# Optimization experiments

Measured on AMD Instinct MI355X. Metric: run time of the kernel, lower is better.

The kernel has to match this reference:

```python
import jax, jax.numpy as jnp
import numpy as np

D_MODEL = 1024
NUM_HEADS = 16
DEPTH = D_MODEL // NUM_HEADS
NEG_INF = -1e9


def setup_inputs() -> dict:
    key = jax.random.key(0)
    ks = jax.random.split(key, 12)
    B, S = 4, 2048
    scale = 1.0 / np.sqrt(D_MODEL)
    inp = {
        "q": jax.random.normal(ks[0], (B, S, D_MODEL), jnp.float32),
        "k": jax.random.normal(ks[1], (B, S, D_MODEL), jnp.float32),
        "v": jax.random.normal(ks[2], (B, S, D_MODEL), jnp.float32),
        "mask": jax.random.randint(ks[3], (B, 1, 1, S), 0, 2, jnp.int32),
        "wq": jax.random.normal(ks[4], (D_MODEL, D_MODEL), jnp.float32) * scale,
        "bq": jnp.zeros((D_MODEL,), jnp.float32),
        "wk": jax.random.normal(ks[5], (D_MODEL, D_MODEL), jnp.float32) * scale,
        "bk": jnp.zeros((D_MODEL,), jnp.float32),
        "wv": jax.random.normal(ks[6], (D_MODEL, D_MODEL), jnp.float32) * scale,
        "bv": jnp.zeros((D_MODEL,), jnp.float32),
        "wo": jax.random.normal(ks[7], (D_MODEL, D_MODEL), jnp.float32) * scale,
        "bo": jnp.zeros((D_MODEL,), jnp.float32),
    }
    return inp


def _split_heads(x):
    # [B, S, D] -> [B, H, S, depth]
    B, S, _ = x.shape
    return x.reshape(B, S, NUM_HEADS, DEPTH).transpose(0, 2, 1, 3)


def reference(q, k, v, mask, wq, bq, wk, bk, wv, bv, wo, bo):
    B, S, _ = q.shape
    qh = _split_heads(q @ wq + bq)  # [B,H,S,d]
    kh = _split_heads(k @ wk + bk)
    vh = _split_heads(v @ wv + bv)
    logits = jnp.einsum("bhqd,bhkd->bhqk", qh, kh) / jnp.sqrt(
        jnp.asarray(DEPTH, jnp.float32))
    logits = logits + mask.astype(jnp.float32) * NEG_INF
    weights = jax.nn.softmax(logits, axis=-1)
    attn = jnp.einsum("bhqk,bhkd->bhqd", weights, vh)
    attn = attn.transpose(0, 2, 1, 3).reshape(B, S, D_MODEL)
    return attn @ wo + bo
```

## Files before the change

### kernel.cpp

```cpp
#include <hip/hip_runtime.h>

#define SB 4
#define SS 2048
#define SD 1024
#define SH 16

typedef float f32x4 __attribute__((ext_vector_type(4)));
typedef __bf16 bf16x8 __attribute__((ext_vector_type(8)));
typedef short short4v __attribute__((ext_vector_type(4)));
typedef unsigned int uint2v __attribute__((ext_vector_type(2)));

__device__ __forceinline__ unsigned short f2bf_(float x) {
    unsigned u = __builtin_bit_cast(unsigned, x);
    unsigned r = u + 0x7FFFu + ((u >> 16) & 1u);
    return (unsigned short)(r >> 16);
}

#define GL2LDS(g, l) __builtin_amdgcn_global_load_lds( \
    (const __attribute__((address_space(1))) unsigned int*)(g), \
    (__attribute__((address_space(3))) unsigned int*)(l), 16, 0, 0)

__global__ __launch_bounds__(256) void maskprep(
        const int* __restrict__ mk, float* __restrict__ MA, int n) {
    int i = blockIdx.x * 256 + threadIdx.x;
    if (i < n)
        MA[i] = (float)mk[i] * (-1e9f * 1.4426950408889634f) - 8.0f;
}

__global__ __launch_bounds__(256) void transpose4(
        const float* __restrict__ w0, const float* __restrict__ w1,
        const float* __restrict__ w2, const float* __restrict__ w3,
        unsigned short* __restrict__ out) {
    __shared__ unsigned short tile[32][33];
    int zz = blockIdx.z;
    const float* src = (zz == 0) ? w0 : (zz == 1) ? w1 : (zz == 2) ? w2 : w3;
    unsigned short* dst = out + (size_t)zz * 1024 * 1024;
    int x = blockIdx.x * 32 + threadIdx.x;
    int y0 = blockIdx.y * 32;
    for (int j = threadIdx.y; j < 32; j += 8)
        tile[j][threadIdx.x] = f2bf_(src[(size_t)(y0 + j) * 1024 + x]);
    __syncthreads();
    int ox = y0 + threadIdx.x;
    int oy0 = blockIdx.x * 32;
    for (int j = threadIdx.y; j < 32; j += 8)
        dst[(size_t)(oy0 + j) * 1024 + ox] = tile[threadIdx.x][j];
}

__global__ __launch_bounds__(256) void gemm_qkv(
        const float* __restrict__ Aq, const float* __restrict__ Ak,
        const float* __restrict__ Avv, const unsigned short* __restrict__ WT,
        const float* __restrict__ bq, const float* __restrict__ bk,
        const float* __restrict__ bv, unsigned short* __restrict__ Qh,
        unsigned short* __restrict__ Kh, unsigned short* __restrict__ VTr,
        float qscl) {
    const int K = 1024, N = 1024;
    __shared__ alignas(16) float Asmf[2][128][32];
    __shared__ alignas(16) unsigned short Bsm[2][128][32];
    const int zone = blockIdx.z;
    const float* Af = (zone == 0) ? Aq : (zone == 1) ? Ak : Avv;
    const unsigned short* BT = WT + (size_t)zone * 1048576;
    const float* bias = (zone == 0) ? bq : (zone == 1) ? bk : bv;

    const int m0 = blockIdx.x * 128, n0 = blockIdx.y * 128;
    const int lane = threadIdx.x & 63, wid = threadIdx.x >> 6;
    const int wr = wid >> 1, wc = wid & 1;
    const int cl = lane & 15, kg = lane >> 4;

    f32x4 acc[4][4] = {};

    auto STAGE = [&](int buf, int k0) {
#pragma unroll
        for (int i = 0; i < 4; ++i) {
            int base = i * 32 + wid * 8;
            int row = base + (lane >> 3);
            int cs = (lane & 7) ^ (row & 7);
            GL2LDS(Af + (size_t)(m0 + row) * K + k0 + cs * 4, &Asmf[buf][base][0]);
        }
#pragma unroll
        for (int i = 0; i < 2; ++i) {
            int base = (i * 4 + wid) * 16;
            int row = base + (lane >> 2);
            int cs = (lane & 3) ^ ((row >> 1) & 3);
            GL2LDS(BT + (size_t)(n0 + row) * K + k0 + cs * 8, &Bsm[buf][base][0]);
        }
    };

    STAGE(0, 0);
    __syncthreads();

    for (int k0 = 0; k0 < K; k0 += 32) {
        int cur = (k0 >> 5) & 1;
        if (k0 + 32 < K) STAGE(cur ^ 1, k0 + 32);

        bf16x8 af[4], bfv[4];
#pragma unroll
        for (int mi = 0; mi < 4; ++mi) {
            int r = wr * 64 + mi * 16 + cl;
            const float* Ar = &Asmf[cur][r][0];
            f32x4 a0 = *(const f32x4*)(Ar + ((2 * kg) ^ (r & 7)) * 4);
            f32x4 a1 = *(const f32x4*)(Ar + ((2 * kg + 1) ^ (r & 7)) * 4);
#pragma unroll
            for (int e = 0; e < 4; ++e) {
                af[mi][e] = (__bf16)a0[e];
                af[mi][4 + e] = (__bf16)a1[e];
            }
        }
#pragma unroll
        for (int ni = 0; ni < 4; ++ni) {
            int r = wc * 64 + ni * 16 + cl;
            bfv[ni] = *(const bf16x8*)&Bsm[cur][r][(kg ^ ((r >> 1) & 3)) * 8];
        }
#pragma unroll
        for (int mi = 0; mi < 4; ++mi)
#pragma unroll
            for (int ni = 0; ni < 4; ++ni)
                acc[mi][ni] = __builtin_amdgcn_mfma_f32_16x16x32_bf16(
                    af[mi], bfv[ni], acc[mi][ni], 0, 0, 0);
        __syncthreads();
    }

    const int rl = (lane >> 4) * 4;
    float os = (zone == 0) ? qscl : 1.0f;
#pragma unroll
    for (int mi = 0; mi < 4; ++mi) {
#pragma unroll
        for (int ni = 0; ni < 4; ++ni) {
            int row = m0 + wr * 64 + mi * 16 + rl;
            int col = n0 + wc * 64 + ni * 16 + cl;
            float bvv = bias[col];
            f32x4 v = acc[mi][ni];
            if (zone < 2) {
                unsigned short* C = (zone == 0) ? Qh : Kh;
#pragma unroll
                for (int j = 0; j < 4; ++j)
                    C[(size_t)(row + j) * N + col] = f2bf_((v[j] + bvv) * os);
            } else {
                int bb = row >> 11, s = row & 2047;
                short4v pk;
#pragma unroll
                for (int j = 0; j < 4; ++j)
                    pk[j] = (short)f2bf_(v[j] + bvv);
                *(short4v*)&VTr[((size_t)(bb * 1024 + col)) * 2048 + s] = pk;
            }
        }
    }
}

__global__ __launch_bounds__(256) void gemm_out(
        const unsigned short* __restrict__ Ab, const unsigned short* __restrict__ BT,
        const float* __restrict__ bias, float* __restrict__ C,
        int M, int N, int K) {
    __shared__ alignas(16) unsigned short Asmb[2][128][32];
    __shared__ alignas(16) unsigned short Bsm[2][128][32];
    const int m0 = blockIdx.x * 128, n0 = blockIdx.y * 128;
    const int lane = threadIdx.x & 63, wid = threadIdx.x >> 6;
    const int wr = wid >> 1, wc = wid & 1;
    const int cl = lane & 15, kg = lane >> 4;

    f32x4 acc[4][4] = {};

    auto STAGE = [&](int buf, int k0) {
#pragma unroll
        for (int i = 0; i < 2; ++i) {
            int base = (i * 4 + wid) * 16;
            int row = base + (lane >> 2);
            int cs = (lane & 3) ^ ((row >> 1) & 3);
            GL2LDS(Ab + (size_t)(m0 + row) * K + k0 + cs * 8, &Asmb[buf][base][0]);
            GL2LDS(BT + (size_t)(n0 + row) * K + k0 + cs * 8, &Bsm[buf][base][0]);
        }
    };

    STAGE(0, 0);
    __syncthreads();

    for (int k0 = 0; k0 < K; k0 += 32) {
        int cur = (k0 >> 5) & 1;
        if (k0 + 32 < K) STAGE(cur ^ 1, k0 + 32);

        bf16x8 af[4], bfv[4];
#pragma unroll
        for (int mi = 0; mi < 4; ++mi) {
            int r = wr * 64 + mi * 16 + cl;
            af[mi] = *(const bf16x8*)&Asmb[cur][r][(kg ^ ((r >> 1) & 3)) * 8];
        }
#pragma unroll
        for (int ni = 0; ni < 4; ++ni) {
            int r = wc * 64 + ni * 16 + cl;
            bfv[ni] = *(const bf16x8*)&Bsm[cur][r][(kg ^ ((r >> 1) & 3)) * 8];
        }
#pragma unroll
        for (int mi = 0; mi < 4; ++mi)
#pragma unroll
            for (int ni = 0; ni < 4; ++ni)
                acc[mi][ni] = __builtin_amdgcn_mfma_f32_16x16x32_bf16(
                    af[mi], bfv[ni], acc[mi][ni], 0, 0, 0);
        __syncthreads();
    }

    const int rl = (lane >> 4) * 4;
#pragma unroll
    for (int mi = 0; mi < 4; ++mi) {
#pragma unroll
        for (int ni = 0; ni < 4; ++ni) {
            int row = m0 + wr * 64 + mi * 16 + rl;
            int col = n0 + wc * 64 + ni * 16 + cl;
            float bv = bias[col];
            f32x4 v = acc[mi][ni];
#pragma unroll
            for (int j = 0; j < 4; ++j)
                C[(size_t)(row + j) * N + col] = v[j] + bv;
        }
    }
}

__global__ __launch_bounds__(512, 4) void attn_kernel(
        const unsigned short* __restrict__ Qp, const unsigned short* __restrict__ Kp,
        const unsigned short* __restrict__ VT, const float* __restrict__ MA,
        unsigned short* __restrict__ O) {
    __shared__ alignas(16) unsigned short Klds[2][128][64];
    __shared__ alignas(16) unsigned short Vlds[2][64][128];
    const int lane = threadIdx.x & 63, wid = threadIdx.x >> 6;
    const int bh = blockIdx.x;
    const int b = bh >> 4, h = bh & 15;
    const int qt = blockIdx.y;
    const int qrow0 = qt * 256 + wid * 32;
    const int cl = lane & 15, kg = lane >> 4;

    bf16x8 qf[2][2];
#pragma unroll
    for (int qh = 0; qh < 2; ++qh)
#pragma unroll
        for (int kh = 0; kh < 2; ++kh)
            qf[qh][kh] = *(const bf16x8*)&Qp[(size_t)(b * SS + qrow0 + qh * 16 + cl) * SD
                                            + h * 64 + kh * 32 + kg * 8];

    const float* MAb = MA + b * SS;

    bf16x8 onesf;
#pragma unroll
    for (int e = 0; e < 8; ++e) onesf[e] = (__bf16)1.0f;

    f32x4 oacc[2][4] = {};
    f32x4 lacc[2] = {};

    auto STAGE = [&](int buf, int tt) {
        int kt = (tt & 15) * 128;
        {
            int r8 = lane >> 3, c8 = lane & 7;
#pragma unroll
            for (int i = 0; i < 2; ++i) {
                int r = i * 64 + wid * 8 + r8;
                int cs = c8 ^ (r & 7);
                GL2LDS(Kp + (size_t)(b * SS + kt + r) * SD + h * 64 + cs * 8,
                       &Klds[buf][i * 64 + wid * 8][0]);
            }
        }
        {
            int r16 = lane >> 4, c16 = lane & 15;
#pragma unroll
            for (int i = 0; i < 2; ++i) {
                int r = i * 32 + wid * 4 + r16;
                int cs = (c16 & 8) | ((c16 & 7) ^ (r & 7));
                GL2LDS(VT + (size_t)(b * 1024 + h * 64 + r) * 2048 + kt + cs * 8,
                       &Vlds[buf][i * 32 + wid * 4][0]);
            }
        }
    };

    auto QKCOL = [&](int buf, int kt, int cf, f32x4* sv) {
        int r = cf * 16 + cl;
        bf16x8 kf0 = *(const bf16x8*)&Klds[buf][r][((0 + kg) ^ (r & 7)) * 8];
        bf16x8 kf1 = *(const bf16x8*)&Klds[buf][r][((4 + kg) ^ (r & 7)) * 8];
        f32x4 M = *(const f32x4*)&MAb[kt + cf * 16 + 4 * kg];
        __builtin_amdgcn_s_setprio(1);
#pragma unroll
        for (int qh = 0; qh < 2; ++qh) {
            f32x4 s = {};
            s = __builtin_amdgcn_mfma_f32_16x16x32_bf16(kf0, qf[qh][0], s, 0, 0, 0);
            s = __builtin_amdgcn_mfma_f32_16x16x32_bf16(kf1, qf[qh][1], s, 0, 0, 0);
#pragma unroll
            for (int j = 0; j < 4; ++j)
                s[j] = __builtin_amdgcn_exp2f(s[j] + M[j]);
            sv[qh] = s;
        }
        __builtin_amdgcn_s_setprio(0);
    };

    auto STEP = [&](int buf, int t) {
        int kt = t * 128;
#pragma unroll
        for (int ks = 0; ks < 4; ++ks) {
            f32x4 sA[2], sB[2];
            QKCOL(buf, kt, ks, sA);
            QKCOL(buf, kt, ks + 4, sB);
            bf16x8 pa[2];
#pragma unroll
            for (int qh = 0; qh < 2; ++qh) {
                pa[qh][0] = (__bf16)sA[qh][0];
                pa[qh][1] = (__bf16)sA[qh][1];
                pa[qh][2] = (__bf16)sA[qh][2];
                pa[qh][3] = (__bf16)sA[qh][3];
                pa[qh][4] = (__bf16)sB[qh][0];
                pa[qh][5] = (__bf16)sB[qh][1];
                pa[qh][6] = (__bf16)sB[qh][2];
                pa[qh][7] = (__bf16)sB[qh][3];
            }
            __builtin_amdgcn_s_setprio(1);
#pragma unroll
            for (int qh = 0; qh < 2; ++qh)
                lacc[qh] = __builtin_amdgcn_mfma_f32_16x16x32_bf16(
                    pa[qh], onesf, lacc[qh], 0, 0, 0);
#pragma unroll
            for (int nf = 0; nf < 4; ++nf) {
                int d = nf * 16 + cl;
                int c16a = 2 * ks + (kg >> 1);
                int c16b = 2 * (ks + 4) + (kg >> 1);
                int cha = (c16a & 8) | ((c16a & 7) ^ (d & 7));
                int chb = (c16b & 8) | ((c16b & 7) ^ (d & 7));
                const char* vb = (const char*)&Vlds[buf][d][0];
                uint2v lo = *(const uint2v*)(vb + cha * 16 + (kg & 1) * 8);
                uint2v hi = *(const uint2v*)(vb + chb * 16 + (kg & 1) * 8);
                bf16x8 vf;
                *(uint2v*)&vf = lo;
                *((uint2v*)&vf + 1) = hi;
#pragma unroll
                for (int qh = 0; qh < 2; ++qh)
                    oacc[qh][nf] = __builtin_amdgcn_mfma_f32_16x16x32_bf16(
                        pa[qh], vf, oacc[qh][nf], 0, 0, 0);
            }
            __builtin_amdgcn_s_setprio(0);
        }
    };

    STAGE(0, 0);
    __syncthreads();
    for (int t = 0; t < 16; ++t) {
        int cur = t & 1;
        STAGE(cur ^ 1, t + 1);
        STEP(cur, t);
        __syncthreads();
    }

#pragma unroll
    for (int qh = 0; qh < 2; ++qh) {
#pragma unroll
        for (int j = 0; j < 4; ++j) {
            float inv = 1.0f / lacc[qh][j];
#pragma unroll
            for (int nf = 0; nf < 4; ++nf)
                O[(size_t)(b * SS + qrow0 + qh * 16 + 4 * kg + j) * SD + h * 64 + nf * 16 + cl] =
                    f2bf_(oacc[qh][nf][j] * inv);
        }
    }
}

extern "C" void kernel_launch(void* const* d_in, const int* in_sizes, int n_in,
                              void* d_out, int out_size, void* d_ws, size_t ws_size,
                              hipStream_t stream) {
    const float* q  = (const float*)d_in[0];
    const float* k  = (const float*)d_in[1];
    const float* v  = (const float*)d_in[2];
    const int*   mk = (const int*)d_in[3];
    const float* wq = (const float*)d_in[4];
    const float* bq = (const float*)d_in[5];
    const float* wk = (const float*)d_in[6];
    const float* bk = (const float*)d_in[7];
    const float* wv = (const float*)d_in[8];
    const float* bv = (const float*)d_in[9];
    const float* wo = (const float*)d_in[10];
    const float* bo = (const float*)d_in[11];
    float* out = (float*)d_out;

    char* ws = (char*)d_ws;
    unsigned short* WT  = (unsigned short*)ws;
    unsigned short* X   = (unsigned short*)(ws + 8388608);
    unsigned short* Qh  = (unsigned short*)(ws + 25165824);
    unsigned short* Kh  = (unsigned short*)(ws + 41943040);
    unsigned short* VTr = (unsigned short*)(ws + 58720256);
    float*          MAf = (float*)(ws + 75497472);

    const float QSCL = 0.125f * 1.4426950408889634f;

    transpose4<<<dim3(32, 32, 4), dim3(32, 8), 0, stream>>>(wq, wk, wv, wo, WT);
    maskprep<<<dim3(32), dim3(256), 0, stream>>>(mk, MAf, SB * SS);

    gemm_qkv<<<dim3(64, 8, 3), dim3(256), 0, stream>>>(
        q, k, v, WT, bq, bk, bv, Qh, Kh, VTr, QSCL);

    attn_kernel<<<dim3(64, 8), dim3(512), 0, stream>>>(Qh, Kh, VTr, MAf, X);

    gemm_out<<<dim3(64, 8), dim3(256), 0, stream>>>(
        X, WT + 3 * 1048576, bo, out, 8192, 1024, 1024);
}
```

Baseline: 206.4 us.

## Shrink attention tiles to 16 query rows per wave and 64-key blocks

Retiles the attention kernel so each wave handles 16 query rows instead of 32 and each iteration stages 64 keys instead of 128. The grid doubles to 1024 blocks. LDS per block halves and register pressure drops, which allows more blocks per CU. The mask is now folded in as the MFMA accumulator init rather than added before exp2. In exchange, K/V tiles are reloaded twice as often per query row, each K fragment is reused by half as many MFMAs, and there are twice as many barrier iterations.

```diff
diff --git a/kernel.cpp b/kernel.cpp
--- a/kernel.cpp
+++ b/kernel.cpp
@@ -213,26 +213,24 @@
     }
 }
 
-__global__ __launch_bounds__(512, 4) void attn_kernel(
+__global__ __launch_bounds__(512) void attn_kernel(
         const unsigned short* __restrict__ Qp, const unsigned short* __restrict__ Kp,
         const unsigned short* __restrict__ VT, const float* __restrict__ MA,
         unsigned short* __restrict__ O) {
-    __shared__ alignas(16) unsigned short Klds[2][128][64];
-    __shared__ alignas(16) unsigned short Vlds[2][64][128];
+    __shared__ alignas(16) unsigned short Klds[2][64][64];
+    __shared__ alignas(16) unsigned short Vlds[2][64][64];
     const int lane = threadIdx.x & 63, wid = threadIdx.x >> 6;
     const int bh = blockIdx.x;
     const int b = bh >> 4, h = bh & 15;
     const int qt = blockIdx.y;
-    const int qrow0 = qt * 256 + wid * 32;
+    const int qrow0 = qt * 128 + wid * 16;
     const int cl = lane & 15, kg = lane >> 4;
 
-    bf16x8 qf[2][2];
-#pragma unroll
-    for (int qh = 0; qh < 2; ++qh)
-#pragma unroll
-        for (int kh = 0; kh < 2; ++kh)
-            qf[qh][kh] = *(const bf16x8*)&Qp[(size_t)(b * SS + qrow0 + qh * 16 + cl) * SD
-                                            + h * 64 + kh * 32 + kg * 8];
+    bf16x8 qf[2];
+#pragma unroll
+    for (int kh = 0; kh < 2; ++kh)
+        qf[kh] = *(const bf16x8*)&Qp[(size_t)(b * SS + qrow0 + cl) * SD
+                                     + h * 64 + kh * 32 + kg * 8];
 
     const float* MAb = MA + b * SS;
 
@@ -240,93 +238,63 @@
 #pragma unroll
     for (int e = 0; e < 8; ++e) onesf[e] = (__bf16)1.0f;
 
-    f32x4 oacc[2][4] = {};
-    f32x4 lacc[2] = {};
+    f32x4 oacc[4] = {};
+    f32x4 lacc = {};
 
     auto STAGE = [&](int buf, int tt) {
-        int kt = (tt & 15) * 128;
-        {
-            int r8 = lane >> 3, c8 = lane & 7;
-#pragma unroll
-            for (int i = 0; i < 2; ++i) {
-                int r = i * 64 + wid * 8 + r8;
-                int cs = c8 ^ (r & 7);
-                GL2LDS(Kp + (size_t)(b * SS + kt + r) * SD + h * 64 + cs * 8,
-                       &Klds[buf][i * 64 + wid * 8][0]);
-            }
-        }
-        {
-            int r16 = lane >> 4, c16 = lane & 15;
-#pragma unroll
-            for (int i = 0; i < 2; ++i) {
-                int r = i * 32 + wid * 4 + r16;
-                int cs = (c16 & 8) | ((c16 & 7) ^ (r & 7));
-                GL2LDS(VT + (size_t)(b * 1024 + h * 64 + r) * 2048 + kt + cs * 8,
-                       &Vlds[buf][i * 32 + wid * 4][0]);
-            }
-        }
-    };
-
-    auto QKCOL = [&](int buf, int kt, int cf, f32x4* sv) {
+        int kt = (tt & 31) * 64;
+        int r = wid * 8 + (lane >> 3);
+        int cs = (lane & 7) ^ (r & 7);
+        GL2LDS(Kp + (size_t)(b * SS + kt + r) * SD + h * 64 + cs * 8,
+               &Klds[buf][wid * 8][0]);
+        GL2LDS(VT + (size_t)(b * 1024 + h * 64 + r) * 2048 + kt + cs * 8,
+               &Vlds[buf][wid * 8][0]);
+    };
+
+    auto QKCOL = [&](int buf, int kt, int cf, f32x4& sv) {
         int r = cf * 16 + cl;
         bf16x8 kf0 = *(const bf16x8*)&Klds[buf][r][((0 + kg) ^ (r & 7)) * 8];
         bf16x8 kf1 = *(const bf16x8*)&Klds[buf][r][((4 + kg) ^ (r & 7)) * 8];
-        f32x4 M = *(const f32x4*)&MAb[kt + cf * 16 + 4 * kg];
+        f32x4 s = *(const f32x4*)&MAb[kt + cf * 16 + 4 * kg];
         __builtin_amdgcn_s_setprio(1);
-#pragma unroll
-        for (int qh = 0; qh < 2; ++qh) {
-            f32x4 s = {};
-            s = __builtin_amdgcn_mfma_f32_16x16x32_bf16(kf0, qf[qh][0], s, 0, 0, 0);
-            s = __builtin_amdgcn_mfma_f32_16x16x32_bf16(kf1, qf[qh][1], s, 0, 0, 0);
-#pragma unroll
-            for (int j = 0; j < 4; ++j)
-                s[j] = __builtin_amdgcn_exp2f(s[j] + M[j]);
-            sv[qh] = s;
-        }
+        s = __builtin_amdgcn_mfma_f32_16x16x32_bf16(kf0, qf[0], s, 0, 0, 0);
+        s = __builtin_amdgcn_mfma_f32_16x16x32_bf16(kf1, qf[1], s, 0, 0, 0);
+#pragma unroll
+        for (int j = 0; j < 4; ++j)
+            s[j] = __builtin_amdgcn_exp2f(s[j]);
         __builtin_amdgcn_s_setprio(0);
+        sv = s;
     };
 
     auto STEP = [&](int buf, int t) {
-        int kt = t * 128;
-#pragma unroll
-        for (int ks = 0; ks < 4; ++ks) {
-            f32x4 sA[2], sB[2];
+        int kt = t * 64;
+#pragma unroll
+        for (int ks = 0; ks < 2; ++ks) {
+            f32x4 sA, sB;
             QKCOL(buf, kt, ks, sA);
-            QKCOL(buf, kt, ks + 4, sB);
-            bf16x8 pa[2];
-#pragma unroll
-            for (int qh = 0; qh < 2; ++qh) {
-                pa[qh][0] = (__bf16)sA[qh][0];
-                pa[qh][1] = (__bf16)sA[qh][1];
-                pa[qh][2] = (__bf16)sA[qh][2];
-                pa[qh][3] = (__bf16)sA[qh][3];
-                pa[qh][4] = (__bf16)sB[qh][0];
-                pa[qh][5] = (__bf16)sB[qh][1];
-                pa[qh][6] = (__bf16)sB[qh][2];
-                pa[qh][7] = (__bf16)sB[qh][3];
-            }
+            QKCOL(buf, kt, ks + 2, sB);
+            bf16x8 pa;
+            pa[0] = (__bf16)sA[0]; pa[1] = (__bf16)sA[1];
+            pa[2] = (__bf16)sA[2]; pa[3] = (__bf16)sA[3];
+            pa[4] = (__bf16)sB[0]; pa[5] = (__bf16)sB[1];
+            pa[6] = (__bf16)sB[2]; pa[7] = (__bf16)sB[3];
             __builtin_amdgcn_s_setprio(1);
-#pragma unroll
-            for (int qh = 0; qh < 2; ++qh)
-                lacc[qh] = __builtin_amdgcn_mfma_f32_16x16x32_bf16(
-                    pa[qh], onesf, lacc[qh], 0, 0, 0);
+            lacc = __builtin_amdgcn_mfma_f32_16x16x32_bf16(pa, onesf, lacc, 0, 0, 0);
 #pragma unroll
             for (int nf = 0; nf < 4; ++nf) {
                 int d = nf * 16 + cl;
                 int c16a = 2 * ks + (kg >> 1);
-                int c16b = 2 * (ks + 4) + (kg >> 1);
-                int cha = (c16a & 8) | ((c16a & 7) ^ (d & 7));
-                int chb = (c16b & 8) | ((c16b & 7) ^ (d & 7));
+                int c16b = c16a + 4;
+                int cha = c16a ^ (d & 7);
+                int chb = c16b ^ (d & 7);
                 const char* vb = (const char*)&Vlds[buf][d][0];
                 uint2v lo = *(const uint2v*)(vb + cha * 16 + (kg & 1) * 8);
                 uint2v hi = *(const uint2v*)(vb + chb * 16 + (kg & 1) * 8);
                 bf16x8 vf;
                 *(uint2v*)&vf = lo;
                 *((uint2v*)&vf + 1) = hi;
-#pragma unroll
-                for (int qh = 0; qh < 2; ++qh)
-                    oacc[qh][nf] = __builtin_amdgcn_mfma_f32_16x16x32_bf16(
-                        pa[qh], vf, oacc[qh][nf], 0, 0, 0);
+                oacc[nf] = __builtin_amdgcn_mfma_f32_16x16x32_bf16(
+                    pa, vf, oacc[nf], 0, 0, 0);
             }
             __builtin_amdgcn_s_setprio(0);
         }
@@ -334,7 +302,7 @@
 
     STAGE(0, 0);
     __syncthreads();
-    for (int t = 0; t < 16; ++t) {
+    for (int t = 0; t < 32; ++t) {
         int cur = t & 1;
         STAGE(cur ^ 1, t + 1);
         STEP(cur, t);
@@ -342,15 +310,12 @@
     }
 
 #pragma unroll
-    for (int qh = 0; qh < 2; ++qh) {
-#pragma unroll
-        for (int j = 0; j < 4; ++j) {
-            float inv = 1.0f / lacc[qh][j];
-#pragma unroll
-            for (int nf = 0; nf < 4; ++nf)
-                O[(size_t)(b * SS + qrow0 + qh * 16 + 4 * kg + j) * SD + h * 64 + nf * 16 + cl] =
-                    f2bf_(oacc[qh][nf][j] * inv);
-        }
+    for (int j = 0; j < 4; ++j) {
+        float inv = 1.0f / lacc[j];
+#pragma unroll
+        for (int nf = 0; nf < 4; ++nf)
+            O[(size_t)(b * SS + qrow0 + 4 * kg + j) * SD + h * 64 + nf * 16 + cl] =
+                f2bf_(oacc[nf][j] * inv);
     }
 }
 
@@ -387,7 +352,7 @@
     gemm_qkv<<<dim3(64, 8, 3), dim3(256), 0, stream>>>(
         q, k, v, WT, bq, bk, bv, Qh, Kh, VTr, QSCL);
 
-    attn_kernel<<<dim3(64, 8), dim3(512), 0, stream>>>(Qh, Kh, VTr, MAf, X);
+    attn_kernel<<<dim3(64, 16), dim3(512), 0, stream>>>(Qh, Kh, VTr, MAf, X);
 
     gemm_out<<<dim3(64, 8), dim3(256), 0, stream>>>(
         X, WT + 3 * 1048576, bo, out, 8192, 1024, 1024);
```

New measurement: 251.4 us. 21.8% more time.
